# Performance work log

Hardware: AMD Instinct MI355X
Metric: run time of the kernel (lower is better)

The kernel has to match this reference:

```python
import jax, jax.numpy as jnp
import numpy as np

B, L, D = 8, 2048, 256
NEG = 10000.0


def setup_inputs() -> dict:
    key = jax.random.key(0)
    kq, kk, kv, km = jax.random.split(key, 4)
    return {
        "query": jax.random.normal(kq, (B, L, D), dtype=jnp.float32),
        "key": jax.random.normal(kk, (B, L, D), dtype=jnp.float32),
        "value": jax.random.normal(kv, (B, L, D), dtype=jnp.float32),
        "mask": jax.random.randint(km, (B, L), 0, 2).astype(bool),
    }


def reference(query, key, value, mask):
    d = query.shape[-1]
    # scores: [B, Lq, Lk]
    e = jnp.einsum("bqd,bkd->bqk", query, key) / jnp.sqrt(jnp.asarray(d, query.dtype))
    # history_only (causal) mask: subtract 10000 where key index > query index
    q_len, k_len = query.shape[1], key.shape[1]
    causal = (jnp.arange(k_len)[None, :] > jnp.arange(q_len)[:, None]).astype(query.dtype)
    e = e - NEG * causal[None, :, :]
    # key padding mask: [B, 1, Lk]
    e = e - NEG * (1.0 - mask.astype(query.dtype))[:, None, :]
    attn = jax.nn.softmax(e, axis=-1)
    return jnp.einsum("bqk,bkd->bqd", attn, value)
```

## Files before the change

kernel.cpp:

```cpp
#include <hip/hip_runtime.h>
#include <stdint.h>

#define NL 2048
#define ND 256
#define KVB 32
#define QB 64
#define NQT 32
#define NT_ALL (NL / KVB)
#define CHUNK 10
#define NCHUNKS_B 125
#define TILE_BYTES (KVB * ND * 2)
#define IMG (8 * NT_ALL * TILE_BYTES)
#define WS_K 256
#define WS_V (WS_K + IMG)
#define WS_P (WS_V + IMG)
#define PART_BYTES (QB * ND * 2 + QB * 8)

typedef __attribute__((ext_vector_type(8))) short short8;
typedef __attribute__((ext_vector_type(4))) short short4v;
typedef __attribute__((ext_vector_type(4))) float f32x4;
typedef __attribute__((ext_vector_type(8))) unsigned short ushort8;

__device__ __forceinline__ unsigned short bf16rne(float x) {
  unsigned u = __builtin_bit_cast(unsigned, x);
  u += 0x7FFFu + ((u >> 16) & 1u);
  return (unsigned short)(u >> 16);
}

__device__ __forceinline__ short8 cvt8(float4 a, float4 b, float scale) {
  short8 v;
  v[0] = (short)bf16rne(a.x * scale);
  v[1] = (short)bf16rne(a.y * scale);
  v[2] = (short)bf16rne(a.z * scale);
  v[3] = (short)bf16rne(a.w * scale);
  v[4] = (short)bf16rne(b.x * scale);
  v[5] = (short)bf16rne(b.y * scale);
  v[6] = (short)bf16rne(b.z * scale);
  v[7] = (short)bf16rne(b.w * scale);
  return v;
}

__global__ void mask_mode_kernel(const unsigned* __restrict__ M, int* __restrict__ flag) {
  bool bad = false;
  for (int i = threadIdx.x; i < 4096; i += 64) {
    if (M[i] > 1u) bad = true;
  }
  unsigned long long b = __ballot(bad);
  if (threadIdx.x == 0) *flag = (b != 0ULL) ? 1 : 0;
}

__global__ __launch_bounds__(128)
void convert_kv(const float* __restrict__ K, const float* __restrict__ V,
                unsigned char* __restrict__ ws) {
  const int t = blockIdx.x;
  const int b = t >> 6, tix = t & 63;
  const float* kt = K + ((size_t)b * NL + tix * KVB) * ND;
  const float* vt = V + ((size_t)b * NL + tix * KVB) * ND;
  unsigned char* kd = ws + WS_K + (size_t)t * TILE_BYTES;
  unsigned char* vd = ws + WS_V + (size_t)t * TILE_BYTES;
#pragma unroll
  for (int it = 0; it < 8; ++it) {
    int idx = it * 128 + threadIdx.x;
    int row = idx >> 5, u = idx & 31, f = u * 8;
    const float4* kp = (const float4*)(kt + (size_t)row * ND + f);
    int kb = (row * 512 + f * 2) ^ ((row & 7) << 4);
    *(short8*)(kd + kb) = cvt8(kp[0], kp[1], 1.0f);
    const float4* vp = (const float4*)(vt + (size_t)row * ND + f);
    int vb = (row >> 2) * 2048 + (u >> 1) * 128 + (row & 3) * 32 + (u & 1) * 16;
    *(short8*)(vd + vb) = cvt8(vp[0], vp[1], 1.0f);
  }
}

__global__ __launch_bounds__(256, 2)
void attn_fwd(const float* __restrict__ Qg, const int* __restrict__ Mg,
              unsigned char* ws, const int* __restrict__ modeFlag) {
  __shared__ unsigned short Ks[2][KVB * ND];
  __shared__ unsigned short Vs[2][KVB * ND];
  __shared__ unsigned short Ps[4][16 * KVB];
  __shared__ float biasC[CHUNK * KVB];

  const int tid = threadIdx.x;
  const int wv = tid >> 6;
  const int lane = tid & 63;
  const int g = lane >> 4;
  const int cc = lane & 15;
  const int maskByteMode = *modeFlag;

  const int fid = blockIdx.x;
  const int b = fid / NCHUNKS_B;
  int rem = fid - b * NCHUNKS_B;
  int qt = 0, c = 0, pbase = 0;
  if (rem < 7) {
    qt = 0; c = rem; pbase = 0;
  } else {
    rem -= 7; pbase = 7;
    for (qt = 1; qt < NQT; ++qt) {
      int ncq = (2 * qt + 2 + CHUNK - 1) / CHUNK;
      if (rem < ncq) { c = rem; break; }
      rem -= ncq; pbase += ncq;
    }
  }
  const int qb = qt * QB;
  const int nt_s = (qt == 0) ? NT_ALL : (2 * qt + 2);
  const int t0 = c * CHUNK;
  const int t1 = min(nt_s, t0 + CHUNK);
  unsigned char* pp = ws + WS_P + (size_t)(b * NCHUNKS_B + pbase + c) * PART_BYTES;
  unsigned short* ppA = (unsigned short*)pp;
  float* ppM = (float*)(pp + QB * ND * 2);
  float* ppL = ppM + QB;

  auto stage_tile = [&](int tix, int bi) {
    const unsigned char* kg = ws + WS_K + ((size_t)(b * NT_ALL + tix)) * TILE_BYTES;
    const unsigned char* vg = ws + WS_V + ((size_t)(b * NT_ALL + tix)) * TILE_BYTES;
#pragma unroll
    for (int s = 0; s < 4; ++s) {
      const int seg = wv * 4 + s;
      __builtin_amdgcn_global_load_lds(
          (const __attribute__((address_space(1))) unsigned int*)(kg + seg * 1024 + lane * 16),
          (__attribute__((address_space(3))) unsigned int*)((unsigned char*)&Ks[bi][0] + seg * 1024),
          16, 0, 0);
      __builtin_amdgcn_global_load_lds(
          (const __attribute__((address_space(1))) unsigned int*)(vg + seg * 1024 + lane * 16),
          (__attribute__((address_space(3))) unsigned int*)((unsigned char*)&Vs[bi][0] + seg * 1024),
          16, 0, 0);
    }
  };

  {
    int nb = (t1 - t0) * KVB;
    for (int i = tid; i < nb; i += 256) {
      size_t gi = (size_t)b * NL + t0 * KVB + i;
      int mv = maskByteMode ? (int)((const unsigned char*)Mg)[gi] : Mg[gi];
      biasC[i] = mv ? 0.f : -10000.f;
    }
  }

  const float* qp = Qg + ((size_t)b * NL + (qb + 16 * wv + cc)) * ND;
  short8 qf[8];
#pragma unroll
  for (int ch = 0; ch < 8; ++ch) {
    int f = ch * 32 + g * 8;
    float4 a0 = *reinterpret_cast<const float4*>(qp + f);
    float4 a1 = *reinterpret_cast<const float4*>(qp + f + 4);
    qf[ch] = cvt8(a0, a1, 0.0625f);
  }

  f32x4 acc[16];
#pragma unroll
  for (int i = 0; i < 16; ++i) acc[i] = (f32x4){0.f, 0.f, 0.f, 0.f};
  float m_run[4], l_run[4];
#pragma unroll
  for (int r = 0; r < 4; ++r) { m_run[r] = -3.0e38f; l_run[r] = 0.f; }

  int buf = 0;
  stage_tile(t0, 0);
  __syncthreads();

  for (int tix = t0; tix < t1; ++tix) {
    if (tix + 1 < t1) stage_tile(tix + 1, buf ^ 1);
    const int kv0 = tix * KVB;
    const float* biasT = &biasC[(tix - t0) * KVB];

    const char* ksB = (const char*)&Ks[buf][0];
    f32x4 s0 = {0.f, 0.f, 0.f, 0.f}, s1 = {0.f, 0.f, 0.f, 0.f};
    __builtin_amdgcn_s_setprio(1);
#pragma unroll
    for (int ch = 0; ch < 8; ++ch) {
      int cbase = ch * 64 + g * 16;
      int b0 = (cc * 512 + cbase) ^ ((cc & 7) << 4);
      int b1 = ((cc + 16) * 512 + cbase) ^ ((cc & 7) << 4);
      short8 k0 = *reinterpret_cast<const short8*>(ksB + b0);
      short8 k1 = *reinterpret_cast<const short8*>(ksB + b1);
      s0 = __builtin_amdgcn_mfma_f32_16x16x32_bf16(qf[ch], k0, s0, 0, 0, 0);
      s1 = __builtin_amdgcn_mfma_f32_16x16x32_bf16(qf[ch], k1, s1, 0, 0, 0);
    }
    __builtin_amdgcn_s_setprio(0);
    float bi0 = biasT[cc], bi1 = biasT[16 + cc];
    s0 += bi0;
    s1 += bi1;
    if (kv0 + KVB - 1 > qb) {
      int kvg0 = kv0 + cc, kvg1 = kv0 + 16 + cc;
      int qg = qb + 16 * wv + 4 * g;
#pragma unroll
      for (int r = 0; r < 4; ++r) {
        if (kvg0 > qg + r) s0[r] -= 10000.f;
        if (kvg1 > qg + r) s1[r] -= 10000.f;
      }
    }
    float rmax[4], rsum[4];
#pragma unroll
    for (int r = 0; r < 4; ++r) rmax[r] = fmaxf(s0[r], s1[r]);
#pragma unroll
    for (int off = 8; off >= 1; off >>= 1) {
#pragma unroll
      for (int r = 0; r < 4; ++r) rmax[r] = fmaxf(rmax[r], __shfl_xor(rmax[r], off));
    }
    bool grow = (rmax[0] > m_run[0] + 8.f) || (rmax[1] > m_run[1] + 8.f) ||
                (rmax[2] > m_run[2] + 8.f) || (rmax[3] > m_run[3] + 8.f);
    if (__any(grow)) {
      f32x4 av;
#pragma unroll
      for (int r = 0; r < 4; ++r) {
        float mn = fmaxf(m_run[r], rmax[r]);
        float alpha = __expf(m_run[r] - mn);
        m_run[r] = mn;
        l_run[r] *= alpha;
        av[r] = alpha;
      }
#pragma unroll
      for (int i = 0; i < 16; ++i) acc[i] *= av;
    }
#pragma unroll
    for (int r = 0; r < 4; ++r) {
      s0[r] = __expf(s0[r] - m_run[r]);
      s1[r] = __expf(s1[r] - m_run[r]);
      rsum[r] = s0[r] + s1[r];
    }
#pragma unroll
    for (int off = 8; off >= 1; off >>= 1) {
#pragma unroll
      for (int r = 0; r < 4; ++r) rsum[r] += __shfl_xor(rsum[r], off);
    }
#pragma unroll
    for (int r = 0; r < 4; ++r) l_run[r] += rsum[r];

    unsigned short* pw = &Ps[wv][0];
#pragma unroll
    for (int r = 0; r < 4; ++r) {
      pw[(4 * g + r) * KVB + cc] = bf16rne(s0[r]);
      pw[(4 * g + r) * KVB + 16 + cc] = bf16rne(s1[r]);
    }
    asm volatile("s_waitcnt lgkmcnt(0)" ::: "memory");
    __builtin_amdgcn_sched_barrier(0);

    short8 pa;
    {
      const unsigned paddr = (unsigned)(uintptr_t)pw + (unsigned)(cc * 64 + g * 16);
      asm volatile("ds_read_b128 %0, %1" : "=&v"(pa) : "v"(paddr) : "memory");
    }
    const unsigned va = (unsigned)(uintptr_t)&Vs[buf][0] + g * 4096 + cc * 8;
    short4v lo[16], hi[16];
#pragma unroll
    for (int ft = 0; ft < 16; ++ft) {
      asm volatile("ds_read_b64_tr_b16 %0, %1 offset:%2"
                   : "=&v"(lo[ft]) : "v"(va), "i"(ft * 128) : "memory");
      asm volatile("ds_read_b64_tr_b16 %0, %1 offset:%2"
                   : "=&v"(hi[ft]) : "v"(va), "i"(ft * 128 + 2048) : "memory");
    }
    asm volatile("s_waitcnt lgkmcnt(15)" ::: "memory");
    __builtin_amdgcn_sched_barrier(0);
    __builtin_amdgcn_s_setprio(1);
#pragma unroll
    for (int ft = 0; ft < 8; ++ft) {
      short8 vb = __builtin_shufflevector(lo[ft], hi[ft], 0, 1, 2, 3, 4, 5, 6, 7);
      acc[ft] = __builtin_amdgcn_mfma_f32_16x16x32_bf16(pa, vb, acc[ft], 0, 0, 0);
    }
    __builtin_amdgcn_s_setprio(0);
    asm volatile("s_waitcnt lgkmcnt(0)" ::: "memory");
    __builtin_amdgcn_sched_barrier(0);
    __builtin_amdgcn_s_setprio(1);
#pragma unroll
    for (int ft = 8; ft < 16; ++ft) {
      short8 vb = __builtin_shufflevector(lo[ft], hi[ft], 0, 1, 2, 3, 4, 5, 6, 7);
      acc[ft] = __builtin_amdgcn_mfma_f32_16x16x32_bf16(pa, vb, acc[ft], 0, 0, 0);
    }
    __builtin_amdgcn_s_setprio(0);

    __syncthreads();
    buf ^= 1;
  }

  unsigned short* sc = &Ks[0][0];
#pragma unroll
  for (int ft = 0; ft < 16; ++ft) {
#pragma unroll
    for (int r = 0; r < 4; ++r) {
      sc[(16 * wv + 4 * g + r) * 256 + ft * 16 + cc] = bf16rne(acc[ft][r]);
    }
  }
  if (cc == 0) {
#pragma unroll
    for (int r = 0; r < 4; ++r) {
      int rr = 16 * wv + 4 * g + r;
      ppM[rr] = m_run[r];
      ppL[rr] = l_run[r];
    }
  }
  __syncthreads();
  {
    const int row = tid >> 2, q4 = tid & 3;
    const unsigned short* srow = sc + row * 256 + q4 * 64;
#pragma unroll
    for (int kk = 0; kk < 8; ++kk) {
      *(ushort8*)(ppA + (size_t)row * ND + q4 * 64 + kk * 8) =
          *(const ushort8*)(srow + kk * 8);
    }
  }
}

__global__ __launch_bounds__(256)
void attn_combine(const unsigned char* __restrict__ ws, float* __restrict__ Og) {
  const int bid = blockIdx.x;
  const int b = bid >> 5, qt = bid & 31;
  const int tid = threadIdx.x;
  const int row = tid >> 2, sub = tid & 3;

  int pbase = 0, nc = 7;
  if (qt > 0) {
    pbase = 7;
    for (int j = 1; j < qt; ++j) pbase += (2 * j + 2 + CHUNK - 1) / CHUNK;
    nc = (2 * qt + 2 + CHUNK - 1) / CHUNK;
  }
  const unsigned char* p0 = ws + WS_P + (size_t)(b * NCHUNKS_B + pbase) * PART_BYTES;

  float M = -3.0e38f;
  for (int c = 0; c < nc; ++c) {
    M = fmaxf(M, *(const float*)(p0 + (size_t)c * PART_BYTES + QB * ND * 2 + row * 4));
  }
  float L = 0.f;
  float o[64];
#pragma unroll
  for (int j = 0; j < 64; ++j) o[j] = 0.f;
  for (int c = 0; c < nc; ++c) {
    const unsigned char* pc = p0 + (size_t)c * PART_BYTES;
    float mm = *(const float*)(pc + QB * ND * 2 + row * 4);
    float ll = *(const float*)(pc + QB * ND * 2 + QB * 4 + row * 4);
    float s = __expf(mm - M);
    L += ll * s;
    const unsigned short* pa =
        (const unsigned short*)pc + (size_t)row * ND + sub * 64;
#pragma unroll
    for (int kk = 0; kk < 8; ++kk) {
      ushort8 a = *(const ushort8*)(pa + kk * 8);
#pragma unroll
      for (int j = 0; j < 8; ++j) {
        unsigned u = ((unsigned)a[j]) << 16;
        o[kk * 8 + j] += __builtin_bit_cast(float, u) * s;
      }
    }
  }
  const float invL = 1.0f / L;
  float* op = Og + ((size_t)b * NL + qt * QB + row) * ND + sub * 64;
#pragma unroll
  for (int kk = 0; kk < 16; ++kk) {
    float4 v = {o[kk * 4] * invL, o[kk * 4 + 1] * invL, o[kk * 4 + 2] * invL,
                o[kk * 4 + 3] * invL};
    *(float4*)(op + kk * 4) = v;
  }
}

extern "C" void kernel_launch(void* const* d_in, const int* in_sizes, int n_in,
                              void* d_out, int out_size, void* d_ws, size_t ws_size,
                              hipStream_t stream) {
  (void)in_sizes; (void)n_in; (void)out_size; (void)ws_size;
  const float* Q = (const float*)d_in[0];
  const float* K = (const float*)d_in[1];
  const float* V = (const float*)d_in[2];
  const int* M = (const int*)d_in[3];
  unsigned char* ws = (unsigned char*)d_ws;

  mask_mode_kernel<<<dim3(1), dim3(64), 0, stream>>>((const unsigned*)M, (int*)ws);
  convert_kv<<<dim3(512), dim3(128), 0, stream>>>(K, V, ws);
  attn_fwd<<<dim3(8 * NCHUNKS_B), dim3(256), 0, stream>>>(Q, M, ws, (const int*)ws);
  attn_combine<<<dim3(256), dim3(256), 0, stream>>>(ws, (float*)d_out);
}
```

Baseline: 109.5 us.

## Single-buffer V, bit-pack mask, raise occupancy, and enlarge KV chunks

Replaces the double-buffered V tile with a single buffer that is loaded after the PV step and overlapped with the next QK step, using explicit vmcnt waits and raw barriers instead of __syncthreads. This shrinks LDS so the launch bound can request 3 blocks per CU. The mask is packed into 32-bit bitmasks by a preparatory kernel, so the per-block bias staging in shared memory goes away. The chunk size grows from 10 to 14 tiles, which gives fewer partials to combine. The cost is fewer, longer blocks and tighter manual synchronization, which carries a risk of races or load imbalance.

```diff
diff --git a/kernel.cpp b/kernel.cpp
--- a/kernel.cpp
+++ b/kernel.cpp
@@ -7,11 +7,12 @@
 #define QB 64
 #define NQT 32
 #define NT_ALL (NL / KVB)
-#define CHUNK 10
-#define NCHUNKS_B 125
+#define CHUNK 14
+#define NCHUNKS_B 94
 #define TILE_BYTES (KVB * ND * 2)
 #define IMG (8 * NT_ALL * TILE_BYTES)
-#define WS_K 256
+#define WS_MB 256
+#define WS_K (WS_MB + 2048)
 #define WS_V (WS_K + IMG)
 #define WS_P (WS_V + IMG)
 #define PART_BYTES (QB * ND * 2 + QB * 8)
@@ -40,13 +41,24 @@
   return v;
 }
 
-__global__ void mask_mode_kernel(const unsigned* __restrict__ M, int* __restrict__ flag) {
+__global__ __launch_bounds__(512)
+void mask_pack(const unsigned* __restrict__ M, unsigned* __restrict__ MB) {
+  __shared__ int badS;
+  if (threadIdx.x == 0) badS = 0;
+  __syncthreads();
   bool bad = false;
-  for (int i = threadIdx.x; i < 4096; i += 64) {
+  for (int i = threadIdx.x; i < 4096; i += 512)
     if (M[i] > 1u) bad = true;
-  }
-  unsigned long long b = __ballot(bad);
-  if (threadIdx.x == 0) *flag = (b != 0ULL) ? 1 : 0;
+  if (__any(bad) && (threadIdx.x & 63) == 0) badS = 1;
+  __syncthreads();
+  const int byteMode = badS;
+  const int i = threadIdx.x;
+  unsigned m = 0;
+  for (int j = 0; j < 32; ++j) {
+    int mv = byteMode ? (int)((const unsigned char*)M)[i * 32 + j] : (int)M[i * 32 + j];
+    m |= (mv ? 1u : 0u) << j;
+  }
+  MB[i] = m;
 }
 
 __global__ __launch_bounds__(128)
@@ -71,29 +83,27 @@
   }
 }
 
-__global__ __launch_bounds__(256, 2)
-void attn_fwd(const float* __restrict__ Qg, const int* __restrict__ Mg,
-              unsigned char* ws, const int* __restrict__ modeFlag) {
+__global__ __launch_bounds__(256, 3)
+void attn_fwd(const float* __restrict__ Qg, const unsigned* __restrict__ MBg,
+              unsigned char* ws) {
   __shared__ unsigned short Ks[2][KVB * ND];
-  __shared__ unsigned short Vs[2][KVB * ND];
+  __shared__ unsigned short Vs[KVB * ND];
   __shared__ unsigned short Ps[4][16 * KVB];
-  __shared__ float biasC[CHUNK * KVB];
 
   const int tid = threadIdx.x;
   const int wv = tid >> 6;
   const int lane = tid & 63;
   const int g = lane >> 4;
   const int cc = lane & 15;
-  const int maskByteMode = *modeFlag;
 
   const int fid = blockIdx.x;
   const int b = fid / NCHUNKS_B;
   int rem = fid - b * NCHUNKS_B;
   int qt = 0, c = 0, pbase = 0;
-  if (rem < 7) {
+  if (rem < 5) {
     qt = 0; c = rem; pbase = 0;
   } else {
-    rem -= 7; pbase = 7;
+    rem -= 5; pbase = 5;
     for (qt = 1; qt < NQT; ++qt) {
       int ncq = (2 * qt + 2 + CHUNK - 1) / CHUNK;
       if (rem < ncq) { c = rem; break; }
@@ -109,9 +119,8 @@
   float* ppM = (float*)(pp + QB * ND * 2);
   float* ppL = ppM + QB;
 
-  auto stage_tile = [&](int tix, int bi) {
+  auto stage_K = [&](int tix, int bi) {
     const unsigned char* kg = ws + WS_K + ((size_t)(b * NT_ALL + tix)) * TILE_BYTES;
-    const unsigned char* vg = ws + WS_V + ((size_t)(b * NT_ALL + tix)) * TILE_BYTES;
 #pragma unroll
     for (int s = 0; s < 4; ++s) {
       const int seg = wv * 4 + s;
@@ -119,21 +128,19 @@
           (const __attribute__((address_space(1))) unsigned int*)(kg + seg * 1024 + lane * 16),
           (__attribute__((address_space(3))) unsigned int*)((unsigned char*)&Ks[bi][0] + seg * 1024),
           16, 0, 0);
+    }
+  };
+  auto stage_V = [&](int tix) {
+    const unsigned char* vg = ws + WS_V + ((size_t)(b * NT_ALL + tix)) * TILE_BYTES;
+#pragma unroll
+    for (int s = 0; s < 4; ++s) {
+      const int seg = wv * 4 + s;
       __builtin_amdgcn_global_load_lds(
           (const __attribute__((address_space(1))) unsigned int*)(vg + seg * 1024 + lane * 16),
-          (__attribute__((address_space(3))) unsigned int*)((unsigned char*)&Vs[bi][0] + seg * 1024),
+          (__attribute__((address_space(3))) unsigned int*)((unsigned char*)&Vs[0] + seg * 1024),
           16, 0, 0);
     }
   };
-
-  {
-    int nb = (t1 - t0) * KVB;
-    for (int i = tid; i < nb; i += 256) {
-      size_t gi = (size_t)b * NL + t0 * KVB + i;
-      int mv = maskByteMode ? (int)((const unsigned char*)Mg)[gi] : Mg[gi];
-      biasC[i] = mv ? 0.f : -10000.f;
-    }
-  }
 
   const float* qp = Qg + ((size_t)b * NL + (qb + 16 * wv + cc)) * ND;
   short8 qf[8];
@@ -152,14 +159,20 @@
 #pragma unroll
   for (int r = 0; r < 4; ++r) { m_run[r] = -3.0e38f; l_run[r] = 0.f; }
 
+  asm volatile("s_waitcnt vmcnt(0)" ::: "memory");
+  stage_K(t0, 0);
+  stage_V(t0);
   int buf = 0;
-  stage_tile(t0, 0);
-  __syncthreads();
 
   for (int tix = t0; tix < t1; ++tix) {
-    if (tix + 1 < t1) stage_tile(tix + 1, buf ^ 1);
+    asm volatile("s_waitcnt vmcnt(4)" ::: "memory");
+    __builtin_amdgcn_sched_barrier(0);
+    __builtin_amdgcn_s_barrier();
+    __builtin_amdgcn_sched_barrier(0);
+    if (tix + 1 < t1) stage_K(tix + 1, buf ^ 1);
+
     const int kv0 = tix * KVB;
-    const float* biasT = &biasC[(tix - t0) * KVB];
+    const unsigned mb = MBg[b * NT_ALL + tix];
 
     const char* ksB = (const char*)&Ks[buf][0];
     f32x4 s0 = {0.f, 0.f, 0.f, 0.f}, s1 = {0.f, 0.f, 0.f, 0.f};
@@ -175,7 +188,8 @@
       s1 = __builtin_amdgcn_mfma_f32_16x16x32_bf16(qf[ch], k1, s1, 0, 0, 0);
     }
     __builtin_amdgcn_s_setprio(0);
-    float bi0 = biasT[cc], bi1 = biasT[16 + cc];
+    float bi0 = ((mb >> cc) & 1u) ? 0.f : -10000.f;
+    float bi1 = ((mb >> (16 + cc)) & 1u) ? 0.f : -10000.f;
     s0 += bi0;
     s1 += bi1;
     if (kv0 + KVB - 1 > qb) {
@@ -230,6 +244,14 @@
       pw[(4 * g + r) * KVB + cc] = bf16rne(s0[r]);
       pw[(4 * g + r) * KVB + 16 + cc] = bf16rne(s1[r]);
     }
+
+    if (tix + 1 < t1) {
+      asm volatile("s_waitcnt vmcnt(4)" ::: "memory");
+    } else {
+      asm volatile("s_waitcnt vmcnt(0)" ::: "memory");
+    }
+    __builtin_amdgcn_sched_barrier(0);
+    __builtin_amdgcn_s_barrier();
     asm volatile("s_waitcnt lgkmcnt(0)" ::: "memory");
     __builtin_amdgcn_sched_barrier(0);
 
@@ -238,7 +260,7 @@
       const unsigned paddr = (unsigned)(uintptr_t)pw + (unsigned)(cc * 64 + g * 16);
       asm volatile("ds_read_b128 %0, %1" : "=&v"(pa) : "v"(paddr) : "memory");
     }
-    const unsigned va = (unsigned)(uintptr_t)&Vs[buf][0] + g * 4096 + cc * 8;
+    const unsigned va = (unsigned)(uintptr_t)&Vs[0] + g * 4096 + cc * 8;
     short4v lo[16], hi[16];
 #pragma unroll
     for (int ft = 0; ft < 16; ++ft) {
@@ -266,7 +288,9 @@
     }
     __builtin_amdgcn_s_setprio(0);
 
-    __syncthreads();
+    __builtin_amdgcn_s_barrier();
+    __builtin_amdgcn_sched_barrier(0);
+    if (tix + 1 < t1) stage_V(tix + 1);
     buf ^= 1;
   }
 
@@ -305,9 +329,9 @@
   const int tid = threadIdx.x;
   const int row = tid >> 2, sub = tid & 3;
 
-  int pbase = 0, nc = 7;
+  int pbase = 0, nc = 5;
   if (qt > 0) {
-    pbase = 7;
+    pbase = 5;
     for (int j = 1; j < qt; ++j) pbase += (2 * j + 2 + CHUNK - 1) / CHUNK;
     nc = (2 * qt + 2 + CHUNK - 1) / CHUNK;
   }
@@ -359,8 +383,10 @@
   const int* M = (const int*)d_in[3];
   unsigned char* ws = (unsigned char*)d_ws;
 
-  mask_mode_kernel<<<dim3(1), dim3(64), 0, stream>>>((const unsigned*)M, (int*)ws);
+  mask_pack<<<dim3(1), dim3(512), 0, stream>>>((const unsigned*)M,
+                                               (unsigned*)(ws + WS_MB));
   convert_kv<<<dim3(512), dim3(128), 0, stream>>>(K, V, ws);
-  attn_fwd<<<dim3(8 * NCHUNKS_B), dim3(256), 0, stream>>>(Q, M, ws, (const int*)ws);
+  attn_fwd<<<dim3(8 * NCHUNKS_B), dim3(256), 0, stream>>>(
+      Q, (const unsigned*)(ws + WS_MB), ws);
   attn_combine<<<dim3(256), dim3(256), 0, stream>>>(ws, (float*)d_out);
 }
```

Measured after the change: 173.2 us. 58.2% more time.

## Transpose QK^T MFMA so P stays in registers; pack mask to bits

Applied to the files above, without the earlier changes.

Swaps the MFMA operand order in the QK^T product so each lane holds scores for one query row. Row max and sum then need only two cross-lane shuffles, and each query row keeps a single running max and sum. The P tile is now packed to bf16 with v_cvt_pk and redistributed by shuffles instead of a write and read through LDS, which removes the Ps buffer and its waitcnt. The key padding mask is packed into bitmasks by a one-block pre-kernel, replacing the per-block float bias array in LDS. In exchange it adds more shuffles, and the data movement on the critical path of the PV MFMA is hard to verify.

```diff
diff --git a/kernel.cpp b/kernel.cpp
--- a/kernel.cpp
+++ b/kernel.cpp
@@ -11,7 +11,8 @@
 #define NCHUNKS_B 125
 #define TILE_BYTES (KVB * ND * 2)
 #define IMG (8 * NT_ALL * TILE_BYTES)
-#define WS_K 256
+#define WS_MB 256
+#define WS_K (WS_MB + 2048)
 #define WS_V (WS_K + IMG)
 #define WS_P (WS_V + IMG)
 #define PART_BYTES (QB * ND * 2 + QB * 8)
@@ -19,6 +20,7 @@
 typedef __attribute__((ext_vector_type(8))) short short8;
 typedef __attribute__((ext_vector_type(4))) short short4v;
 typedef __attribute__((ext_vector_type(4))) float f32x4;
+typedef __attribute__((ext_vector_type(4))) unsigned int u32x4;
 typedef __attribute__((ext_vector_type(8))) unsigned short ushort8;
 
 __device__ __forceinline__ unsigned short bf16rne(float x) {
@@ -40,13 +42,24 @@
   return v;
 }
 
-__global__ void mask_mode_kernel(const unsigned* __restrict__ M, int* __restrict__ flag) {
+__global__ __launch_bounds__(512)
+void mask_pack(const unsigned* __restrict__ M, unsigned* __restrict__ MB) {
+  __shared__ int badS;
+  if (threadIdx.x == 0) badS = 0;
+  __syncthreads();
   bool bad = false;
-  for (int i = threadIdx.x; i < 4096; i += 64) {
+  for (int i = threadIdx.x; i < 4096; i += 512)
     if (M[i] > 1u) bad = true;
-  }
-  unsigned long long b = __ballot(bad);
-  if (threadIdx.x == 0) *flag = (b != 0ULL) ? 1 : 0;
+  if (__any(bad) && (threadIdx.x & 63) == 0) badS = 1;
+  __syncthreads();
+  const int byteMode = badS;
+  const int i = threadIdx.x;
+  unsigned m = 0;
+  for (int j = 0; j < 32; ++j) {
+    int mv = byteMode ? (int)((const unsigned char*)M)[i * 32 + j] : (int)M[i * 32 + j];
+    m |= (mv ? 1u : 0u) << j;
+  }
+  MB[i] = m;
 }
 
 __global__ __launch_bounds__(128)
@@ -72,19 +85,16 @@
 }
 
 __global__ __launch_bounds__(256, 2)
-void attn_fwd(const float* __restrict__ Qg, const int* __restrict__ Mg,
-              unsigned char* ws, const int* __restrict__ modeFlag) {
+void attn_fwd(const float* __restrict__ Qg, const unsigned* __restrict__ MBg,
+              unsigned char* ws) {
   __shared__ unsigned short Ks[2][KVB * ND];
   __shared__ unsigned short Vs[2][KVB * ND];
-  __shared__ unsigned short Ps[4][16 * KVB];
-  __shared__ float biasC[CHUNK * KVB];
 
   const int tid = threadIdx.x;
   const int wv = tid >> 6;
   const int lane = tid & 63;
   const int g = lane >> 4;
   const int cc = lane & 15;
-  const int maskByteMode = *modeFlag;
 
   const int fid = blockIdx.x;
   const int b = fid / NCHUNKS_B;
@@ -126,15 +136,6 @@
     }
   };
 
-  {
-    int nb = (t1 - t0) * KVB;
-    for (int i = tid; i < nb; i += 256) {
-      size_t gi = (size_t)b * NL + t0 * KVB + i;
-      int mv = maskByteMode ? (int)((const unsigned char*)Mg)[gi] : Mg[gi];
-      biasC[i] = mv ? 0.f : -10000.f;
-    }
-  }
-
   const float* qp = Qg + ((size_t)b * NL + (qb + 16 * wv + cc)) * ND;
   short8 qf[8];
 #pragma unroll
@@ -144,13 +145,12 @@
     float4 a1 = *reinterpret_cast<const float4*>(qp + f + 4);
     qf[ch] = cvt8(a0, a1, 0.0625f);
   }
+  const int qg = qb + 16 * wv + cc;
 
   f32x4 acc[16];
 #pragma unroll
   for (int i = 0; i < 16; ++i) acc[i] = (f32x4){0.f, 0.f, 0.f, 0.f};
-  float m_run[4], l_run[4];
-#pragma unroll
-  for (int r = 0; r < 4; ++r) { m_run[r] = -3.0e38f; l_run[r] = 0.f; }
+  float m_run = -3.0e38f, l_run = 0.f;
 
   int buf = 0;
   stage_tile(t0, 0);
@@ -159,7 +159,7 @@
   for (int tix = t0; tix < t1; ++tix) {
     if (tix + 1 < t1) stage_tile(tix + 1, buf ^ 1);
     const int kv0 = tix * KVB;
-    const float* biasT = &biasC[(tix - t0) * KVB];
+    const unsigned mb = MBg[b * NT_ALL + tix];
 
     const char* ksB = (const char*)&Ks[buf][0];
     f32x4 s0 = {0.f, 0.f, 0.f, 0.f}, s1 = {0.f, 0.f, 0.f, 0.f};
@@ -171,73 +171,68 @@
       int b1 = ((cc + 16) * 512 + cbase) ^ ((cc & 7) << 4);
       short8 k0 = *reinterpret_cast<const short8*>(ksB + b0);
       short8 k1 = *reinterpret_cast<const short8*>(ksB + b1);
-      s0 = __builtin_amdgcn_mfma_f32_16x16x32_bf16(qf[ch], k0, s0, 0, 0, 0);
-      s1 = __builtin_amdgcn_mfma_f32_16x16x32_bf16(qf[ch], k1, s1, 0, 0, 0);
+      s0 = __builtin_amdgcn_mfma_f32_16x16x32_bf16(k0, qf[ch], s0, 0, 0, 0);
+      s1 = __builtin_amdgcn_mfma_f32_16x16x32_bf16(k1, qf[ch], s1, 0, 0, 0);
     }
     __builtin_amdgcn_s_setprio(0);
-    float bi0 = biasT[cc], bi1 = biasT[16 + cc];
-    s0 += bi0;
-    s1 += bi1;
-    if (kv0 + KVB - 1 > qb) {
-      int kvg0 = kv0 + cc, kvg1 = kv0 + 16 + cc;
-      int qg = qb + 16 * wv + 4 * g;
-#pragma unroll
-      for (int r = 0; r < 4; ++r) {
-        if (kvg0 > qg + r) s0[r] -= 10000.f;
-        if (kvg1 > qg + r) s1[r] -= 10000.f;
-      }
-    }
-    float rmax[4], rsum[4];
-#pragma unroll
-    for (int r = 0; r < 4; ++r) rmax[r] = fmaxf(s0[r], s1[r]);
-#pragma unroll
-    for (int off = 8; off >= 1; off >>= 1) {
-#pragma unroll
-      for (int r = 0; r < 4; ++r) rmax[r] = fmaxf(rmax[r], __shfl_xor(rmax[r], off));
-    }
-    bool grow = (rmax[0] > m_run[0] + 8.f) || (rmax[1] > m_run[1] + 8.f) ||
-                (rmax[2] > m_run[2] + 8.f) || (rmax[3] > m_run[3] + 8.f);
+
+#pragma unroll
+    for (int r = 0; r < 4; ++r) {
+      int k0i = 4 * g + r, k1i = 16 + 4 * g + r;
+      if (!((mb >> k0i) & 1u)) s0[r] -= 10000.f;
+      if (!((mb >> k1i) & 1u)) s1[r] -= 10000.f;
+      if (kv0 + k0i > qg) s0[r] -= 10000.f;
+      if (kv0 + k1i > qg) s1[r] -= 10000.f;
+    }
+
+    float rmax = fmaxf(fmaxf(fmaxf(s0[0], s0[1]), fmaxf(s0[2], s0[3])),
+                       fmaxf(fmaxf(s1[0], s1[1]), fmaxf(s1[2], s1[3])));
+    rmax = fmaxf(rmax, __shfl_xor(rmax, 16));
+    rmax = fmaxf(rmax, __shfl_xor(rmax, 32));
+    bool grow = (rmax > m_run + 8.f);
     if (__any(grow)) {
+      float mn = fmaxf(m_run, rmax);
+      float alpha = __expf(m_run - mn);
+      m_run = mn;
+      l_run *= alpha;
       f32x4 av;
 #pragma unroll
-      for (int r = 0; r < 4; ++r) {
-        float mn = fmaxf(m_run[r], rmax[r]);
-        float alpha = __expf(m_run[r] - mn);
-        m_run[r] = mn;
-        l_run[r] *= alpha;
-        av[r] = alpha;
-      }
+      for (int r = 0; r < 4; ++r) av[r] = __shfl(alpha, 20 * g + r);
 #pragma unroll
       for (int i = 0; i < 16; ++i) acc[i] *= av;
     }
+    float p0[4], p1[4];
 #pragma unroll
     for (int r = 0; r < 4; ++r) {
-      s0[r] = __expf(s0[r] - m_run[r]);
-      s1[r] = __expf(s1[r] - m_run[r]);
-      rsum[r] = s0[r] + s1[r];
-    }
-#pragma unroll
-    for (int off = 8; off >= 1; off >>= 1) {
-#pragma unroll
-      for (int r = 0; r < 4; ++r) rsum[r] += __shfl_xor(rsum[r], off);
-    }
-#pragma unroll
-    for (int r = 0; r < 4; ++r) l_run[r] += rsum[r];
-
-    unsigned short* pw = &Ps[wv][0];
-#pragma unroll
-    for (int r = 0; r < 4; ++r) {
-      pw[(4 * g + r) * KVB + cc] = bf16rne(s0[r]);
-      pw[(4 * g + r) * KVB + 16 + cc] = bf16rne(s1[r]);
-    }
-    asm volatile("s_waitcnt lgkmcnt(0)" ::: "memory");
-    __builtin_amdgcn_sched_barrier(0);
-
-    short8 pa;
-    {
-      const unsigned paddr = (unsigned)(uintptr_t)pw + (unsigned)(cc * 64 + g * 16);
-      asm volatile("ds_read_b128 %0, %1" : "=&v"(pa) : "v"(paddr) : "memory");
-    }
+      p0[r] = __expf(s0[r] - m_run);
+      p1[r] = __expf(s1[r] - m_run);
+    }
+    float rsum = (p0[0] + p0[1]) + (p0[2] + p0[3]) +
+                 (p1[0] + p1[1]) + (p1[2] + p1[3]);
+    rsum += __shfl_xor(rsum, 16);
+    rsum += __shfl_xor(rsum, 32);
+    l_run += rsum;
+
+    unsigned a0, a1, b0w, b1w;
+    asm("v_cvt_pk_bf16_f32 %0, %1, %2" : "=v"(a0) : "v"(p0[0]), "v"(p0[1]));
+    asm("v_cvt_pk_bf16_f32 %0, %1, %2" : "=v"(a1) : "v"(p0[2]), "v"(p0[3]));
+    asm("v_cvt_pk_bf16_f32 %0, %1, %2" : "=v"(b0w) : "v"(p1[0]), "v"(p1[1]));
+    asm("v_cvt_pk_bf16_f32 %0, %1, %2" : "=v"(b1w) : "v"(p1[2]), "v"(p1[3]));
+    const int srcLo = cc + ((g & 1) << 5);
+    const int srcHi = srcLo + 16;
+    unsigned wa0 = (unsigned)__shfl((int)a0, srcLo);
+    unsigned wa1 = (unsigned)__shfl((int)a1, srcLo);
+    unsigned wa2 = (unsigned)__shfl((int)a0, srcHi);
+    unsigned wa3 = (unsigned)__shfl((int)a1, srcHi);
+    unsigned wb0 = (unsigned)__shfl((int)b0w, srcLo);
+    unsigned wb1 = (unsigned)__shfl((int)b1w, srcLo);
+    unsigned wb2 = (unsigned)__shfl((int)b0w, srcHi);
+    unsigned wb3 = (unsigned)__shfl((int)b1w, srcHi);
+    const bool hiHalf = (g >= 2);
+    u32x4 paw = {hiHalf ? wb0 : wa0, hiHalf ? wb1 : wa1,
+                 hiHalf ? wb2 : wa2, hiHalf ? wb3 : wa3};
+    short8 pa = __builtin_bit_cast(short8, paw);
+
     const unsigned va = (unsigned)(uintptr_t)&Vs[buf][0] + g * 4096 + cc * 8;
     short4v lo[16], hi[16];
 #pragma unroll
@@ -278,13 +273,9 @@
       sc[(16 * wv + 4 * g + r) * 256 + ft * 16 + cc] = bf16rne(acc[ft][r]);
     }
   }
-  if (cc == 0) {
-#pragma unroll
-    for (int r = 0; r < 4; ++r) {
-      int rr = 16 * wv + 4 * g + r;
-      ppM[rr] = m_run[r];
-      ppL[rr] = l_run[r];
-    }
+  if (g == 0) {
+    ppM[16 * wv + cc] = m_run;
+    ppL[16 * wv + cc] = l_run;
   }
   __syncthreads();
   {
@@ -359,8 +350,10 @@
   const int* M = (const int*)d_in[3];
   unsigned char* ws = (unsigned char*)d_ws;
 
-  mask_mode_kernel<<<dim3(1), dim3(64), 0, stream>>>((const unsigned*)M, (int*)ws);
+  mask_pack<<<dim3(1), dim3(512), 0, stream>>>((const unsigned*)M,
+                                               (unsigned*)(ws + WS_MB));
   convert_kv<<<dim3(512), dim3(128), 0, stream>>>(K, V, ws);
-  attn_fwd<<<dim3(8 * NCHUNKS_B), dim3(256), 0, stream>>>(Q, M, ws, (const int*)ws);
+  attn_fwd<<<dim3(8 * NCHUNKS_B), dim3(256), 0, stream>>>(
+      Q, (const unsigned*)(ws + WS_MB), ws);
   attn_combine<<<dim3(256), dim3(256), 0, stream>>>(ws, (float*)d_out);
 }
```

Result: faster. 103.1 us (-5.8%).
